# Kernel optimization log

Hardware: AMD Instinct MI355X
Metric: run time of the kernel (lower is better)

## Reference

```python
import jax, jax.numpy as jnp
import numpy as np

N_ORDER = 256      # HiPPO order (window_size=[256])
OUT_LEN = 96       # output_window_size
IN_LEN = 720       # input_window_size
MULTISCALE = [1, 2, 4]
MODES = 32         # min(32, min(OUT_LEN, IN_LEN)//2)
EPS = 1e-5


def _transition(N):
    Q = np.arange(N, dtype=np.float64)
    R = (2 * Q + 1)[:, None]
    j, i = np.meshgrid(Q, Q)
    A = np.where(i < j, -1.0, (-1.0) ** (i - j + 1)) * R
    B = (-1.0) ** Q[:, None] * R
    return A, B


def _bilinear_discretize(A, B, dt):
    # scipy cont2discrete(method='bilinear'): Ad = (I - dt/2 A)^-1 (I + dt/2 A), Bd = (I - dt/2 A)^-1 dt B
    n = A.shape[0]
    I = np.eye(n)
    ima = I - 0.5 * dt * A
    Ad = np.linalg.solve(ima, I + 0.5 * dt * A)
    Bd = np.linalg.solve(ima, dt * B)
    return Ad, Bd.squeeze(-1)


def _eval_legendre(N, x):
    # Legendre P_n(x), n=0..N-1, via three-term recurrence. Returns [len(x), N].
    P = np.zeros((N, x.shape[0]))
    P[0] = 1.0
    if N > 1:
        P[1] = x
    for n in range(1, N - 1):
        P[n + 1] = ((2 * n + 1) * x * P[n] - n * P[n - 1]) / (n + 1)
    return P.T


def setup_inputs() -> dict:
    key = jax.random.key(0)
    ks = jax.random.split(key, 4)
    B, L, E = 16, IN_LEN, 64
    x = jax.random.normal(ks[0], (B, L, E), dtype=jnp.float32)
    scale = 1.0 / (N_ORDER * N_ORDER)
    wr = scale * jax.random.uniform(ks[1], (3, N_ORDER, N_ORDER, MODES), dtype=jnp.float32)
    wi = scale * jax.random.uniform(ks[2], (3, N_ORDER, N_ORDER, MODES), dtype=jnp.float32)
    mlp_w = 0.1 * jax.random.normal(ks[3], (1, 3), dtype=jnp.float32)
    mlp_b = jnp.zeros((1,), dtype=jnp.float32)
    A_c, B_c = _transition(N_ORDER)
    Ads, Bds, evs = [], [], []
    for m in MULTISCALE:
        dt = 1.0 / OUT_LEN / m
        Ad, Bd = _bilinear_discretize(A_c, B_c, dt)
        vals = np.arange(0.0, 1.0, dt)
        ev = _eval_legendre(N_ORDER, 1.0 - 2.0 * vals)  # [m*OUT_LEN, N]
        Ads.append(Ad); Bds.append(Bd); evs.append(ev[-OUT_LEN:])
    A = jnp.asarray(np.stack(Ads), dtype=jnp.float32)          # [3,N,N]
    Bv = jnp.asarray(np.stack(Bds), dtype=jnp.float32)         # [3,N]
    eval_last = jnp.asarray(np.stack(evs), dtype=jnp.float32)  # [3,OUT_LEN,N]
    return {"x": x, "wr": wr, "wi": wi, "mlp_w": mlp_w, "mlp_b": mlp_b,
            "A": A, "Bv": Bv, "eval_last": eval_last}


def _hippo(xin, Ad, Bd):
    # xin: [B,E,T] -> states [B,E,N,T]; c_t = A c_{t-1} + B f_t
    c0 = jnp.zeros(xin.shape[:2] + (Ad.shape[0],), xin.dtype)
    def step(c, f):  # f: [B,E]
        c = c @ Ad.T + f[..., None] * Bd
        return c, c
    _, cs = jax.lax.scan(step, c0, jnp.moveaxis(xin, -1, 0))  # [T,B,E,N]
    return jnp.transpose(cs, (1, 2, 3, 0))


def _spec_conv(xc, wr, wi):
    # xc: [B,E,N,T]; FFT -> low-mode complex channel mix -> iFFT
    T = xc.shape[-1]
    x_ft = jnp.fft.rfft(xc)                 # [B,E,N,T//2+1]
    a = x_ft[..., :MODES]
    w = (wr + 1j * wi).astype(a.dtype)      # [N,N,MODES]
    out = jnp.einsum('bjix,iox->bjox', a, w)
    nf = T // 2 + 1
    out_ft = jnp.pad(out, ((0, 0), (0, 0), (0, 0), (0, nf - MODES)))
    return jnp.fft.irfft(out_ft, n=T)       # [B,E,N,T]


def reference(x, wr, wi, mlp_w, mlp_b, A, Bv, eval_last):
    # instance standard scale (RevIN-style, no affine)
    mean = jnp.mean(x, axis=1, keepdims=True)            # [B,1,E]
    std = jnp.sqrt(jnp.var(x, axis=1, keepdims=True) + EPS)
    xn = (x - mean) / std
    xe = jnp.transpose(xn, (0, 2, 1))                    # [B,E,L]
    decs = []
    for s, m in enumerate(MULTISCALE):
        T = m * OUT_LEN
        x_in = xe[:, :, -T:]
        xc = _hippo(x_in, A[s], Bv[s])                   # [B,E,N,T]
        out1 = _spec_conv(xc, wr[s], wi[s])              # [B,E,N,T]
        x_dec_c = out1[:, :, :, OUT_LEN - 1]             # [B,E,N]  (input >= output branch, jump_dist=0)
        decs.append(x_dec_c @ eval_last[s].T)            # [B,E,OUT_LEN]
    xd = jnp.stack(decs, axis=-1)                        # [B,E,OUT,3]
    xd = (xd @ mlp_w.T + mlp_b)[..., 0]                  # [B,E,OUT]
    xd = jnp.transpose(xd, (0, 2, 1))                    # [B,OUT,E]
    return xd * std + mean
```

## Files before the change

kernel.cpp:

```cpp
#include <hip/hip_runtime.h>

typedef unsigned short u16;
typedef unsigned int u32;

typedef __bf16 bf16x8 __attribute__((ext_vector_type(8)));
typedef unsigned short ushort8 __attribute__((ext_vector_type(8)));
typedef float f32x16 __attribute__((ext_vector_type(16)));

#define STATSP 2048
#define EPOFF 32768
#define KKOFF0 591872
#define KKOFF1 616448
#define KKOFF2 665600
#define WOFF 763904
#define R0OFF 5482496
#define R1OFF 6072320
#define R2OFF 7251968
#define HTOTOFF 11675648
#define AD64 0
#define PD64 196608
#define KKD64 786432

__device__ __forceinline__ u32 pack_hl(float a) {
  u32 bits = __builtin_bit_cast(u32, a);
  u32 hi = (bits + 0x7fffu + ((bits >> 16) & 1u)) >> 16;
  float hif = __builtin_bit_cast(float, hi << 16);
  float r = a - hif;
  u32 lo = __builtin_bit_cast(u32, r) >> 16;
  return hi | (lo << 16);
}

__device__ __forceinline__ void unpk8(const u32* p, bf16x8& h, bf16x8& l) {
  ushort8 hu, lu;
#pragma unroll
  for (int j = 0; j < 8; ++j) {
    u32 v = p[j];
    hu[j] = (unsigned short)(v & 0xffffu);
    lu[j] = (unsigned short)(v >> 16);
  }
  h = __builtin_bit_cast(bf16x8, hu);
  l = __builtin_bit_cast(bf16x8, lu);
}

__device__ __forceinline__ void gload_lds16(const float* g, float* l) {
  __builtin_amdgcn_global_load_lds(
      (const __attribute__((address_space(1))) void*)g,
      (__attribute__((address_space(3))) void*)l, 16, 0, 0);
}

__global__ __launch_bounds__(256) void k_pre(const float* __restrict__ Ab,
                                             const float* __restrict__ Bb,
                                             const float* __restrict__ xin,
                                             const float* __restrict__ ev,
                                             float* __restrict__ ws) {
  __shared__ float rs[4][64], rq[4][64];
  int blk = blockIdx.x, tid = threadIdx.x;
  if (blk < 771) {
    double* dws = (double*)(ws + WOFF);
    int idx = blk * 256 + tid;
    if (idx < 196608) {
      dws[AD64 + idx] = (double)Ab[idx];
    } else {
      int g = idx - 196608;
      const int rowoff[3] = {0, 24576, 73728};
      int s = g >> 8, i = g & 255;
      dws[KKD64 + rowoff[s] + i] = (double)Bb[g];
    }
  } else if (blk < 963) {
    int b2 = blk - 771;
    int b = b2 / 12, part = b2 % 12;
    int j = tid & 63, g = tid >> 6;
    const float* xp = xin + ((size_t)b * 720 + part * 60 + g) * 64 + j;
    float sum = 0.f, ss = 0.f;
#pragma unroll
    for (int i = 0; i < 15; ++i) {
      float v = xp[(size_t)i * 256];
      sum += v; ss += v * v;
    }
    rs[g][j] = sum; rq[g][j] = ss;
    __syncthreads();
    if (g == 0) {
      float s = rs[0][j] + rs[1][j] + rs[2][j] + rs[3][j];
      float q = rq[0][j] + rq[1][j] + rq[2][j] + rq[3][j];
      float* dst = ws + STATSP + ((size_t)b2 * 64 + j) * 2;
      dst[0] = s; dst[1] = q;
    }
  } else if (blk < 987) {
    int idx = (blk - 963) * 256 + tid;
    for (; idx < 36864; idx += 24 * 256) ws[HTOTOFF + idx] = 0.f;
  } else if (blk < 1275) {
    int idx = (blk - 987) * 256 + tid;
    u32 ph = pack_hl(ev[idx]);
    u16* eb = (u16*)((u32*)ws + EPOFF);
    eb[idx] = (u16)(ph & 0xffffu);
    eb[73728 + idx] = (u16)(ph >> 16);
  } else if (blk < 1467) {
    int g0 = ((blk - 1275) * 256 + tid) * 4;
    int s = g0 >> 16, off = g0 & 65535;
    double* dst = (double*)(ws + WOFF) + PD64 + (size_t)(s * 3) * 65536 + off;
    dst[0] = 0.; dst[1] = 0.; dst[2] = 0.; dst[3] = 0.;
  } else {
    int g0 = ((blk - 1467) * 256 + tid) * 4;
    int local = (g0 < 24576) ? g0 : (g0 < 73728 ? g0 - 24576 : g0 - 73728);
    if (local >= 256) {
      double* dst = (double*)(ws + WOFF) + KKD64 + g0;
      dst[0] = 0.; dst[1] = 0.; dst[2] = 0.; dst[3] = 0.;
    }
  }
}

struct CJobs {
  const double* A[12]; const double* B[12]; double* C[12];
  int M[12]; int transB[12]; int tile0[12];
  int njobs;
};

__global__ __launch_bounds__(256) void k_chain(CJobs jb) {
  int bid = blockIdx.x;
  int j = 0;
  for (int q = 1; q < jb.njobs; ++q) if (bid >= jb.tile0[q]) j = q;
  int local = bid - jb.tile0[j];
  int tB = jb.transB[j];
  int tid = threadIdx.x;
  if (tB == 2) {
    double* Z = jb.C[j] + (size_t)local * 1024 + tid * 4;
    Z[0] = 0.; Z[1] = 0.; Z[2] = 0.; Z[3] = 0.;
    return;
  }
  int M = jb.M[j];
  const double* A = jb.A[j];
  const double* Bm = jb.B[j];
  double* C = jb.C[j];
  int kq = local & 3, tn = (local >> 2) & 7, tm = local >> 5;
  int row0 = tm * 32, col0 = tn * 32, k0 = kq * 64;
  __shared__ double As[32][65];
  __shared__ double Bs[64][33];
  {
    int r = tid >> 3, k8 = (tid & 7) << 3;
    if (row0 + r < M) {
      const double* src = A + (size_t)(row0 + r) * 256 + k0 + k8;
#pragma unroll
      for (int u = 0; u < 8; ++u) As[r][k8 + u] = src[u];
    } else {
#pragma unroll
      for (int u = 0; u < 8; ++u) As[r][k8 + u] = 0.0;
    }
  }
  if (tB == 0) {
    int k = tid >> 2, c8 = (tid & 3) << 3;
    const double* src = Bm + (size_t)(k0 + k) * 256 + col0 + c8;
#pragma unroll
    for (int u = 0; u < 8; ++u) Bs[k][c8 + u] = src[u];
  } else {
    int c = tid >> 3, k8 = (tid & 7) << 3;
    const double* src = Bm + (size_t)(col0 + c) * 256 + k0 + k8;
#pragma unroll
    for (int u = 0; u < 8; ++u) Bs[k8 + u][c] = src[u];
  }
  __syncthreads();
  int ty = tid >> 4, tx = tid & 15;
  double a00 = 0., a01 = 0., a10 = 0., a11 = 0.;
#pragma unroll 8
  for (int k = 0; k < 64; ++k) {
    double x0 = As[2 * ty][k], x1 = As[2 * ty + 1][k];
    double y0 = Bs[k][2 * tx], y1 = Bs[k][2 * tx + 1];
    a00 = fma(x0, y0, a00); a01 = fma(x0, y1, a01);
    a10 = fma(x1, y0, a10); a11 = fma(x1, y1, a11);
  }
  int r0 = row0 + 2 * ty, c0 = col0 + 2 * tx;
  if (r0 < M) {
    __hip_atomic_fetch_add(&C[(size_t)r0 * 256 + c0], a00, __ATOMIC_RELAXED, __HIP_MEMORY_SCOPE_AGENT);
    __hip_atomic_fetch_add(&C[(size_t)r0 * 256 + c0 + 1], a01, __ATOMIC_RELAXED, __HIP_MEMORY_SCOPE_AGENT);
  }
  if (r0 + 1 < M) {
    __hip_atomic_fetch_add(&C[(size_t)(r0 + 1) * 256 + c0], a10, __ATOMIC_RELAXED, __HIP_MEMORY_SCOPE_AGENT);
    __hip_atomic_fetch_add(&C[(size_t)(r0 + 1) * 256 + c0 + 1], a11, __ATOMIC_RELAXED, __HIP_MEMORY_SCOPE_AGENT);
  }
}

__global__ __launch_bounds__(256) void k_pack(float* __restrict__ ws) {
  int idx = blockIdx.x * 256 + threadIdx.x;
  const double* KD = (const double*)(ws + WOFF) + KKD64;
  const int kko[3] = {KKOFF0, KKOFF1, KKOFF2};
  int s, local;
  if (idx < 24576) { s = 0; local = idx; }
  else if (idx < 73728) { s = 1; local = idx - 24576; }
  else { s = 2; local = idx - 73728; }
  ((u32*)ws)[kko[s] + local] = pack_hl((float)KD[idx]);
}

__global__ __launch_bounds__(384, 5) void k_s3(const float* __restrict__ wr,
                                               const float* __restrict__ wi,
                                               float* __restrict__ ws) {
  __shared__ float stage[2][2048];
  __shared__ u32 pairs[3 * 1056];
  int bid = blockIdx.x;
  int jidx = bid >> 7;
  int r127 = bid & 127;
  int mb = ((r127 & 7) << 4) | (r127 >> 3);
  int s = jidx >> 1, p = jidx & 1;
  const float* w = (p ? wi : wr) + (size_t)s * 2097152;
  const u16* ebase = (const u16*)((const u32*)ws + EPOFF);
  const u16* eh = ebase + (size_t)s * 24576;
  const u16* el = ebase + 73728 + (size_t)s * 24576;
  int i0 = mb * 2;
  int tid = threadIdx.x;
  int lane = tid & 63;
  int wid = tid >> 6;
  int il = wid & 1, f = wid >> 1;

  int tcol = lane & 31;
  int og8 = (lane >> 5) << 3;
  const u16* bhp = eh + (size_t)(f * 32 + tcol) * 256 + og8;
  const u16* blp = el + (size_t)(f * 32 + tcol) * 256 + og8;

  bool stager = (wid < 4);
  int sq0 = wid * 2;
  int s_i[2], s_o[2], s_x[2];
#pragma unroll
  for (int j = 0; j < 2; ++j) {
    int qq = sq0 + j;
    s_i[j] = qq >> 2;
    s_o[j] = (qq & 3) * 8 + (lane >> 3);
    s_x[j] = (lane & 7) * 4;
  }

  f32x16 acc;
#pragma unroll
  for (int r = 0; r < 16; ++r) acc[r] = 0.f;

  if (stager) {
#pragma unroll
    for (int j = 0; j < 2; ++j) {
      const float* g = w + (((size_t)(i0 + s_i[j]) * 256 + s_o[j]) << 5) + s_x[j];
      gload_lds16(g, &stage[0][(sq0 + j) * 256]);
    }
  }
  __syncthreads();

#pragma unroll 2
  for (int c = 0; c < 8; ++c) {
    int buf = c & 1;
    if (c < 7 && stager) {
      int kon = (c + 1) * 32;
#pragma unroll
      for (int j = 0; j < 2; ++j) {
        const float* g = w + (((size_t)(i0 + s_i[j]) * 256 + kon + s_o[j]) << 5) + s_x[j];
        gload_lds16(g, &stage[buf ^ 1][(sq0 + j) * 256]);
      }
    }
    int ko = c * 32;
#pragma unroll
    for (int ks = 0; ks < 2; ++ks) {
      int ob = ks * 16 + og8;
      float fa[8];
#pragma unroll
      for (int j = 0; j < 8; ++j)
        fa[j] = stage[buf][il * 1024 + (ob + j) * 32 + tcol];
      bf16x8 ah, al;
#pragma unroll
      for (int j = 0; j < 8; ++j) {
        __bf16 h = (__bf16)fa[j];
        ah[j] = h;
        al[j] = (__bf16)(fa[j] - (float)h);
      }
      bf16x8 bh = *(const bf16x8*)(bhp + ko + ks * 16);
      bf16x8 bl = *(const bf16x8*)(blp + ko + ks * 16);
      acc = __builtin_amdgcn_mfma_f32_32x32x16_bf16(ah, bh, acc, 0, 0, 0);
      acc = __builtin_amdgcn_mfma_f32_32x32x16_bf16(ah, bl, acc, 0, 0, 0);
      acc = __builtin_amdgcn_mfma_f32_32x32x16_bf16(al, bh, acc, 0, 0, 0);
    }
    __syncthreads();
  }

  int x0 = (lane >> 5) << 2;
  u32 mine[16];
#pragma unroll
  for (int r = 0; r < 16; ++r) mine[r] = pack_hl(acc[r]);
  if (il == 0) {
#pragma unroll
    for (int r = 0; r < 16; ++r) {
      int row = x0 + (r & 3) + ((r >> 2) << 3);
      pairs[f * 1056 + row * 33 + tcol] = mine[r];
    }
  }
  __syncthreads();
  if (il == 1) {
    u32* W2 = (u32*)(ws + WOFF) + (size_t)jidx * 786432 +
              (size_t)(mb >> 2) * 24576 + ((mb & 3) << 1);
#pragma unroll
    for (int r = 0; r < 16; ++r) {
      int row = x0 + (r & 3) + ((r >> 2) << 3);
      uint2 st;
      st.x = pairs[f * 1056 + row * 33 + tcol];
      st.y = mine[r];
      *(uint2*)(W2 + (size_t)(row * 96 + f * 32 + tcol) * 8) = st;
    }
  }
}

__global__ __launch_bounds__(256) void k_s4(float* __restrict__ ws) {
  int bid = blockIdx.x;
  const int cums[6] = {0, 36, 72, 144, 216, 360};
  int jidx = 0;
#pragma unroll
  for (int q = 1; q < 6; ++q) if (bid >= cums[q]) jidx = q;
  int local = bid - cums[jidx];
  int s = jidx >> 1, p = jidx & 1;
  const int Ts[3] = {96, 192, 384};
  const int KKo[3] = {KKOFF0, KKOFF1, KKOFF2};
  const int Ro[3] = {R0OFF, R1OFF, R2OFF};
  int T = Ts[s];
  int td = local / 12, tn = local % 12;
  int d0 = td * 32;
  int tid = threadIdx.x;
  int lane = tid & 63, wid = tid >> 6;
  int n0 = tn * 256 + wid * 64;
  int l31 = lane & 31, kg = lane >> 5;
  const u32* Ap = (const u32*)ws + KKo[s] + (size_t)(d0 + l31) * 256 + kg * 8;
  const u32* Bp = (const u32*)ws + WOFF + (size_t)jidx * 786432 + (size_t)kg * 24576;
  const u32* b0p = Bp + (size_t)(n0 + l31) * 8;
  const u32* b1p = Bp + (size_t)(n0 + 32 + l31) * 8;
  float* C = ws + Ro[s] + (size_t)p * T * 3072;

  f32x16 acc0, acc1;
#pragma unroll
  for (int r = 0; r < 16; ++r) { acc0[r] = 0.f; acc1[r] = 0.f; }

#pragma unroll 2
  for (int ks = 0; ks < 16; ++ks) {
    uint4 a0 = *(const uint4*)(Ap + ks * 16);
    uint4 a1 = *(const uint4*)(Ap + ks * 16 + 4);
    size_t bo = (size_t)ks * 49152;
    uint4 x0 = *(const uint4*)(b0p + bo);
    uint4 x1 = *(const uint4*)(b0p + bo + 4);
    uint4 y0 = *(const uint4*)(b1p + bo);
    uint4 y1 = *(const uint4*)(b1p + bo + 4);
    u32 ap[8] = {a0.x, a0.y, a0.z, a0.w, a1.x, a1.y, a1.z, a1.w};
    bf16x8 ah, al;
    unpk8(ap, ah, al);
    {
      u32 bp[8] = {x0.x, x0.y, x0.z, x0.w, x1.x, x1.y, x1.z, x1.w};
      bf16x8 bh, bl;
      unpk8(bp, bh, bl);
      acc0 = __builtin_amdgcn_mfma_f32_32x32x16_bf16(ah, bh, acc0, 0, 0, 0);
      acc0 = __builtin_amdgcn_mfma_f32_32x32x16_bf16(ah, bl, acc0, 0, 0, 0);
      acc0 = __builtin_amdgcn_mfma_f32_32x32x16_bf16(al, bh, acc0, 0, 0, 0);
      acc0 = __builtin_amdgcn_mfma_f32_32x32x16_bf16(al, bl, acc0, 0, 0, 0);
    }
    {
      u32 bp[8] = {y0.x, y0.y, y0.z, y0.w, y1.x, y1.y, y1.z, y1.w};
      bf16x8 bh, bl;
      unpk8(bp, bh, bl);
      acc1 = __builtin_amdgcn_mfma_f32_32x32x16_bf16(ah, bh, acc1, 0, 0, 0);
      acc1 = __builtin_amdgcn_mfma_f32_32x32x16_bf16(ah, bl, acc1, 0, 0, 0);
      acc1 = __builtin_amdgcn_mfma_f32_32x32x16_bf16(al, bh, acc1, 0, 0, 0);
      acc1 = __builtin_amdgcn_mfma_f32_32x32x16_bf16(al, bl, acc1, 0, 0, 0);
    }
  }

  int crow = kg << 2;
#pragma unroll
  for (int r = 0; r < 16; ++r) {
    int row = d0 + crow + (r & 3) + ((r >> 2) << 3);
    C[(size_t)row * 3072 + n0 + l31] = acc0[r];
    C[(size_t)row * 3072 + n0 + 32 + l31] = acc1[r];
  }
}

__global__ __launch_bounds__(192) void k_s5a(const float* __restrict__ mlpw, float* __restrict__ ws) {
  int bid = blockIdx.x;
  int s = bid >> 7;
  int rem = bid & 127;
  int x = rem >> 2;
  int tq = rem & 3;
  const int Ts[3] = {96, 192, 384};
  const int Ro[3] = {R0OFF, R1OFF, R2OFF};
  const int lpbase[3] = {288, 192, 0};
  int T = Ts[s];
  int Lc = T >> 3;
  __shared__ float cs[384][2];
  __shared__ float Lsr[8][24], Lsi[8][24];
  int tid = threadIdx.x;
  for (int e = tid; e < T; e += 192) {
    float th = 6.283185307179586f * (float)e / (float)T;
    cs[e][0] = cosf(th);
    cs[e][1] = sinf(th);
  }
  int c = tid / 24, tl = tid % 24;
  int t = tq * 24 + tl;
  const float* Rre = ws + Ro[s] + (size_t)x * 96 + t;
  const float* Rim = Rre + (size_t)T * 3072;
  float* Htot = ws + HTOTOFF;
  float wsc = mlpw[s];
  __syncthreads();
  int d0 = c * Lc;
  float zr = 0.f, zi = 0.f;
  for (int d = d0; d < d0 + Lc; ++d) {
    float rr = Rre[(size_t)d * 3072];
    float ri = Rim[(size_t)d * 3072];
    int e1 = (x * d) % T;
    float c1 = cs[e1][0], s1 = cs[e1][1];
    zr += c1 * rr + s1 * ri;
    zi += c1 * ri - s1 * rr;
  }
  Lsr[c][tl] = zr; Lsi[c][tl] = zi;
  __syncthreads();
  if (c == 0) {
    float pr = 0.f, pi = 0.f;
#pragma unroll
    for (int cc = 0; cc < 8; ++cc) {
      float lr = Lsr[cc][tl], li = Lsi[cc][tl];
      Lsr[cc][tl] = pr; Lsi[cc][tl] = pi;
      pr += lr; pi += li;
    }
  }
  __syncthreads();
  zr = Lsr[c][tl]; zi = Lsi[c][tl];
  float sc = (((x == 0) ? 1.f : 2.f) / (float)T) * wsc;
  for (int d = d0; d < d0 + Lc; ++d) {
    float rr = Rre[(size_t)d * 3072];
    float ri = Rim[(size_t)d * 3072];
    int e1 = (x * d) % T;
    float c1 = cs[e1][0], s1 = cs[e1][1];
    zr += c1 * rr + s1 * ri;
    zi += c1 * ri - s1 * rr;
    int k = T - 1 - d;
    int e2 = (x * (95 - k)) % T;
    if (e2 < 0) e2 += T;
    float c2 = cs[e2][0], s2 = cs[e2][1];
    atomicAdd(Htot + (size_t)(lpbase[s] + k) * 96 + t, sc * (c2 * zr - s2 * zi));
  }
}

__global__ __launch_bounds__(256) void k_s6(const float* __restrict__ xin, const float* __restrict__ mlpb_p,
                                            const float* __restrict__ ws, float* __restrict__ out) {
  int b = blockIdx.x >> 2, tq = blockIdx.x & 3;
  int tid = threadIdx.x;
  int j = tid & 63, tsub = tid >> 6;
  __shared__ float Ht[384 * 24];
  for (int idx = tid; idx < 384 * 24; idx += 256) {
    int lp = idx / 24, c = idx % 24;
    Ht[idx] = ws[HTOTOFF + lp * 96 + tq * 24 + c];
  }
  float ssum = 0.f, sq = 0.f;
#pragma unroll
  for (int p = 0; p < 12; ++p) {
    const float* src = ws + STATSP + (((size_t)b * 12 + p) * 64 + j) * 2;
    ssum += src[0]; sq += src[1];
  }
  float mn = ssum * (1.f / 720.f);
  float var = sq * (1.f / 720.f) - mn * mn;
  float sd = sqrtf(var + 1e-5f);
  __syncthreads();
  float mlpb = mlpb_p[0];
  float acc[6] = {0.f, 0.f, 0.f, 0.f, 0.f, 0.f};
  float accS[6] = {0.f, 0.f, 0.f, 0.f, 0.f, 0.f};
  const float* xp = xin + ((size_t)b * 720 + 336) * 64 + j;
  for (int lp = 0; lp < 384; ++lp) {
    float xv = xp[(size_t)lp * 64];
    const float* hr = &Ht[lp * 24 + tsub * 6];
    float2 h01 = *(const float2*)&hr[0];
    float2 h23 = *(const float2*)&hr[2];
    float2 h45 = *(const float2*)&hr[4];
    float hh[6] = {h01.x, h01.y, h23.x, h23.y, h45.x, h45.y};
#pragma unroll
    for (int u = 0; u < 6; ++u) {
      acc[u] += xv * hh[u];
      accS[u] += hh[u];
    }
  }
#pragma unroll
  for (int u = 0; u < 6; ++u) {
    int t = tq * 24 + tsub * 6 + u;
    float val = acc[u] + mn * (1.f - accS[u]) + sd * mlpb;
    out[((size_t)b * 96 + t) * 64 + j] = val;
  }
}

extern "C" void kernel_launch(void* const* d_in, const int* in_sizes, int n_in,
                              void* d_out, int out_size, void* d_ws, size_t ws_size,
                              hipStream_t stream) {
  const float* x  = (const float*)d_in[0];
  const float* wr = (const float*)d_in[1];
  const float* wi = (const float*)d_in[2];
  const float* mw = (const float*)d_in[3];
  const float* mb = (const float*)d_in[4];
  const float* Ab = (const float*)d_in[5];
  const float* Bb = (const float*)d_in[6];
  const float* ev = (const float*)d_in[7];
  float* wsf = (float*)d_ws;
  float* out = (float*)d_out;

  k_pre<<<1635, 256, 0, stream>>>(Ab, Bb, x, ev, wsf);

  const double* AD = (const double*)(wsf + WOFF) + AD64;
  double* PD = (double*)(wsf + WOFF) + PD64;
  double* KD = (double*)(wsf + WOFF) + KKD64;
  static const int Ts[3] = {96, 192, 384};
  static const int rowoff[3] = {0, 24576, 73728};

  int have[3] = {1, 1, 1};
  for (int r = 0; r <= 8; ++r) {
    CJobs jb;
    jb.njobs = 0;
    int tiles = 0;
    for (int s = 0; s < 3; ++s) {
      int T = Ts[s];
      if (have[s] >= T) continue;
      const double* Pn = (r == 0) ? (AD + (size_t)s * 65536)
                                  : (PD + (size_t)(s * 3 + (r - 1) % 3) * 65536);
      int M = ((2 * have[s] < T) ? 2 * have[s] : T) - have[s];
      int q = jb.njobs++;
      jb.A[q] = KD + rowoff[s]; jb.B[q] = Pn;
      jb.C[q] = KD + rowoff[s] + (size_t)have[s] * 256;
      jb.M[q] = M; jb.transB[q] = 1; jb.tile0[q] = tiles;
      tiles += ((M + 31) / 32) * 32;
      if (2 * have[s] < T) {
        q = jb.njobs++;
        jb.A[q] = Pn; jb.B[q] = Pn;
        jb.C[q] = PD + (size_t)(s * 3 + r % 3) * 65536;
        jb.M[q] = 256; jb.transB[q] = 0; jb.tile0[q] = tiles;
        tiles += 256;
        if (4 * have[s] < T) {
          q = jb.njobs++;
          jb.A[q] = nullptr; jb.B[q] = nullptr;
          jb.C[q] = PD + (size_t)(s * 3 + (r + 1) % 3) * 65536;
          jb.M[q] = 0; jb.transB[q] = 2; jb.tile0[q] = tiles;
          tiles += 64;
        }
      }
      have[s] = (2 * have[s] < T) ? 2 * have[s] : T;
    }
    if (jb.njobs) k_chain<<<tiles, 256, 0, stream>>>(jb);
  }

  k_pack<<<672, 256, 0, stream>>>(wsf);
  k_s3<<<768, 384, 0, stream>>>(wr, wi, wsf);
  k_s4<<<504, 256, 0, stream>>>(wsf);
  k_s5a<<<384, 192, 0, stream>>>(mw, wsf);
  k_s6<<<64, 256, 0, stream>>>(x, mb, wsf, out);
}
```

Before: 330.4 us.

## Split s5 prefix-sum stage into two kernels and widen s6 grid

The s5 stage becomes two kernels. A partial-sum kernel writes per-chunk complex sums to scratch, and a final kernel does an exclusive prefix over the prior chunks before applying the atomic scatter. This replaces the in-block shared-memory scan and doubles the block count, using 16 chunks instead of 8 with unrolled templated loops. Separately, k_s6 is launched with 12 t-chunks per batch instead of 4, tripling its blocks for better CU occupancy on the small launch. The cost is one extra launch, a scratch round-trip, and redundant reloading of the Ht table per block.

```diff
diff --git a/kernel.cpp b/kernel.cpp
--- a/kernel.cpp
+++ b/kernel.cpp
@@ -16,6 +16,7 @@
 #define R0OFF 5482496
 #define R1OFF 6072320
 #define R2OFF 7251968
+#define SCROFF 9611264
 #define HTOTOFF 11675648
 #define AD64 0
 #define PD64 196608
@@ -368,35 +369,15 @@
   }
 }
 
-__global__ __launch_bounds__(192) void k_s5a(const float* __restrict__ mlpw, float* __restrict__ ws) {
-  int bid = blockIdx.x;
-  int s = bid >> 7;
-  int rem = bid & 127;
-  int x = rem >> 2;
-  int tq = rem & 3;
-  const int Ts[3] = {96, 192, 384};
-  const int Ro[3] = {R0OFF, R1OFF, R2OFF};
-  const int lpbase[3] = {288, 192, 0};
-  int T = Ts[s];
-  int Lc = T >> 3;
-  __shared__ float cs[384][2];
-  __shared__ float Lsr[8][24], Lsi[8][24];
-  int tid = threadIdx.x;
-  for (int e = tid; e < T; e += 192) {
-    float th = 6.283185307179586f * (float)e / (float)T;
-    cs[e][0] = cosf(th);
-    cs[e][1] = sinf(th);
-  }
-  int c = tid / 24, tl = tid % 24;
-  int t = tq * 24 + tl;
-  const float* Rre = ws + Ro[s] + (size_t)x * 96 + t;
-  const float* Rim = Rre + (size_t)T * 3072;
-  float* Htot = ws + HTOTOFF;
-  float wsc = mlpw[s];
-  __syncthreads();
-  int d0 = c * Lc;
-  float zr = 0.f, zi = 0.f;
-  for (int d = d0; d < d0 + Lc; ++d) {
+
+template <int LC, int T>
+__device__ __forceinline__ void s5_partial(const float* __restrict__ Rre,
+                                           const float* __restrict__ Rim,
+                                           const float (*cs)[2], int x, int d0,
+                                           float& zr, float& zi) {
+#pragma unroll
+  for (int u = 0; u < LC; ++u) {
+    int d = d0 + u;
     float rr = Rre[(size_t)d * 3072];
     float ri = Rim[(size_t)d * 3072];
     int e1 = (x * d) % T;
@@ -404,21 +385,17 @@
     zr += c1 * rr + s1 * ri;
     zi += c1 * ri - s1 * rr;
   }
-  Lsr[c][tl] = zr; Lsi[c][tl] = zi;
-  __syncthreads();
-  if (c == 0) {
-    float pr = 0.f, pi = 0.f;
-#pragma unroll
-    for (int cc = 0; cc < 8; ++cc) {
-      float lr = Lsr[cc][tl], li = Lsi[cc][tl];
-      Lsr[cc][tl] = pr; Lsi[cc][tl] = pi;
-      pr += lr; pi += li;
-    }
-  }
-  __syncthreads();
-  zr = Lsr[c][tl]; zi = Lsi[c][tl];
-  float sc = (((x == 0) ? 1.f : 2.f) / (float)T) * wsc;
-  for (int d = d0; d < d0 + Lc; ++d) {
+}
+
+template <int LC, int T>
+__device__ __forceinline__ void s5_final(const float* __restrict__ Rre,
+                                         const float* __restrict__ Rim,
+                                         const float (*cs)[2], int x, int d0,
+                                         float zr, float zi, float sc,
+                                         float* __restrict__ Hdst, int t) {
+#pragma unroll
+  for (int u = 0; u < LC; ++u) {
+    int d = d0 + u;
     float rr = Rre[(size_t)d * 3072];
     float ri = Rim[(size_t)d * 3072];
     int e1 = (x * d) % T;
@@ -429,19 +406,85 @@
     int e2 = (x * (95 - k)) % T;
     if (e2 < 0) e2 += T;
     float c2 = cs[e2][0], s2 = cs[e2][1];
-    atomicAdd(Htot + (size_t)(lpbase[s] + k) * 96 + t, sc * (c2 * zr - s2 * zi));
-  }
+    atomicAdd(Hdst + (size_t)k * 96 + t, sc * (c2 * zr - s2 * zi));
+  }
+}
+
+__global__ __launch_bounds__(192, 2) void k_s5p(float* __restrict__ ws) {
+  int bid = blockIdx.x;
+  int s = bid >> 8;
+  int rem = bid & 255;
+  int x = rem >> 3;
+  int cpair = rem & 7;
+  const int Ts[3] = {96, 192, 384};
+  const int Ro[3] = {R0OFF, R1OFF, R2OFF};
+  int T = Ts[s];
+  __shared__ float cs[384][2];
+  int tid = threadIdx.x;
+  for (int e = tid; e < T; e += 192) {
+    float th = 6.283185307179586f * (float)e / (float)T;
+    cs[e][0] = cosf(th);
+    cs[e][1] = sinf(th);
+  }
+  int ch = cpair * 2 + (tid >= 96);
+  int t = tid - ((tid >= 96) ? 96 : 0);
+  const float* Rre = ws + Ro[s] + (size_t)x * 96 + t;
+  const float* Rim = Rre + (size_t)T * 3072;
+  __syncthreads();
+  float zr = 0.f, zi = 0.f;
+  if (s == 0)      s5_partial<6, 96>(Rre, Rim, cs, x, ch * 6, zr, zi);
+  else if (s == 1) s5_partial<12, 192>(Rre, Rim, cs, x, ch * 12, zr, zi);
+  else             s5_partial<24, 384>(Rre, Rim, cs, x, ch * 24, zr, zi);
+  float* SCR = ws + SCROFF + (((size_t)(s * 32 + x) * 16 + ch) * 96 + t) * 2;
+  SCR[0] = zr; SCR[1] = zi;
+}
+
+__global__ __launch_bounds__(192, 2) void k_s5f(const float* __restrict__ mlpw,
+                                                float* __restrict__ ws) {
+  int bid = blockIdx.x;
+  int s = bid >> 8;
+  int rem = bid & 255;
+  int x = rem >> 3;
+  int cpair = rem & 7;
+  const int Ts[3] = {96, 192, 384};
+  const int Ro[3] = {R0OFF, R1OFF, R2OFF};
+  const int lpbase[3] = {288, 192, 0};
+  int T = Ts[s];
+  __shared__ float cs[384][2];
+  int tid = threadIdx.x;
+  for (int e = tid; e < T; e += 192) {
+    float th = 6.283185307179586f * (float)e / (float)T;
+    cs[e][0] = cosf(th);
+    cs[e][1] = sinf(th);
+  }
+  int ch = cpair * 2 + (tid >= 96);
+  int t = tid - ((tid >= 96) ? 96 : 0);
+  const float* Rre = ws + Ro[s] + (size_t)x * 96 + t;
+  const float* Rim = Rre + (size_t)T * 3072;
+  const float* SCR = ws + SCROFF + ((size_t)(s * 32 + x) * 16 * 96 + t) * 2;
+  float zr = 0.f, zi = 0.f;
+  for (int cc = 0; cc < ch; ++cc) {
+    zr += SCR[(size_t)cc * 192];
+    zi += SCR[(size_t)cc * 192 + 1];
+  }
+  float wsc = mlpw[s];
+  float sc = (((x == 0) ? 1.f : 2.f) / (float)T) * wsc;
+  float* Hdst = ws + HTOTOFF + (size_t)lpbase[s] * 96;
+  __syncthreads();
+  if (s == 0)      s5_final<6, 96>(Rre, Rim, cs, x, ch * 6, zr, zi, sc, Hdst, t);
+  else if (s == 1) s5_final<12, 192>(Rre, Rim, cs, x, ch * 12, zr, zi, sc, Hdst, t);
+  else             s5_final<24, 384>(Rre, Rim, cs, x, ch * 24, zr, zi, sc, Hdst, t);
 }
 
 __global__ __launch_bounds__(256) void k_s6(const float* __restrict__ xin, const float* __restrict__ mlpb_p,
                                             const float* __restrict__ ws, float* __restrict__ out) {
-  int b = blockIdx.x >> 2, tq = blockIdx.x & 3;
+  int b = blockIdx.x / 12, tc = blockIdx.x % 12;
   int tid = threadIdx.x;
   int j = tid & 63, tsub = tid >> 6;
-  __shared__ float Ht[384 * 24];
-  for (int idx = tid; idx < 384 * 24; idx += 256) {
-    int lp = idx / 24, c = idx % 24;
-    Ht[idx] = ws[HTOTOFF + lp * 96 + tq * 24 + c];
+  __shared__ float Ht[384 * 8];
+  for (int idx = tid; idx < 384 * 8; idx += 256) {
+    int lp = idx >> 3, c = idx & 7;
+    Ht[idx] = ws[HTOTOFF + lp * 96 + tc * 8 + c];
   }
   float ssum = 0.f, sq = 0.f;
 #pragma unroll
@@ -454,28 +497,17 @@
   float sd = sqrtf(var + 1e-5f);
   __syncthreads();
   float mlpb = mlpb_p[0];
-  float acc[6] = {0.f, 0.f, 0.f, 0.f, 0.f, 0.f};
-  float accS[6] = {0.f, 0.f, 0.f, 0.f, 0.f, 0.f};
+  float acc0 = 0.f, acc1 = 0.f, accS0 = 0.f, accS1 = 0.f;
   const float* xp = xin + ((size_t)b * 720 + 336) * 64 + j;
   for (int lp = 0; lp < 384; ++lp) {
     float xv = xp[(size_t)lp * 64];
-    const float* hr = &Ht[lp * 24 + tsub * 6];
-    float2 h01 = *(const float2*)&hr[0];
-    float2 h23 = *(const float2*)&hr[2];
-    float2 h45 = *(const float2*)&hr[4];
-    float hh[6] = {h01.x, h01.y, h23.x, h23.y, h45.x, h45.y};
-#pragma unroll
-    for (int u = 0; u < 6; ++u) {
-      acc[u] += xv * hh[u];
-      accS[u] += hh[u];
-    }
-  }
-#pragma unroll
-  for (int u = 0; u < 6; ++u) {
-    int t = tq * 24 + tsub * 6 + u;
-    float val = acc[u] + mn * (1.f - accS[u]) + sd * mlpb;
-    out[((size_t)b * 96 + t) * 64 + j] = val;
-  }
+    float2 h = *(const float2*)&Ht[lp * 8 + tsub * 2];
+    acc0 += xv * h.x; accS0 += h.x;
+    acc1 += xv * h.y; accS1 += h.y;
+  }
+  int t = tc * 8 + tsub * 2;
+  out[((size_t)b * 96 + t) * 64 + j] = acc0 + mn * (1.f - accS0) + sd * mlpb;
+  out[((size_t)b * 96 + t + 1) * 64 + j] = acc1 + mn * (1.f - accS1) + sd * mlpb;
 }
 
 extern "C" void kernel_launch(void* const* d_in, const int* in_sizes, int n_in,
@@ -538,6 +570,7 @@
   k_pack<<<672, 256, 0, stream>>>(wsf);
   k_s3<<<768, 384, 0, stream>>>(wr, wi, wsf);
   k_s4<<<504, 256, 0, stream>>>(wsf);
-  k_s5a<<<384, 192, 0, stream>>>(mw, wsf);
-  k_s6<<<64, 256, 0, stream>>>(x, mb, wsf, out);
-}
+  k_s5p<<<768, 192, 0, stream>>>(wsf);
+  k_s5f<<<768, 192, 0, stream>>>(mw, wsf);
+  k_s6<<<192, 256, 0, stream>>>(x, mb, wsf, out);
+}
```

New measurement: 316.7 us. 1.04x faster.
